# Kernel optimization log

Measured on AMD Instinct MI355X. Metric: run time of the kernel, lower is better.

The kernel has to match this reference:

```python
import jax, jax.numpy as jnp
import numpy as np

EMBED_DIM = 512
BLOCK = 511
N_HEAD = 8
N_GLOBAL = 4
N_LOCAL = 2
N_MIX = 2
RECEP = 4
T = 2 * BLOCK + 2  # [task, clip, BLOCK upper, BLOCK lower]
HD = EMBED_DIM // N_HEAD
NEG = -1e9


def _build_masks():
    bs = BLOCK
    temporal = np.concatenate([np.zeros(2), np.arange(bs) * 2 + 1, np.arange(bs) * 2 + 2])
    seq = temporal[None, :] <= temporal[:, None]  # causal over interleaved temporal order
    tq = np.concatenate([np.arange(bs) * 2 + 1 - 2 * RECEP + 1] * 2)
    tk = np.concatenate([np.arange(bs) * 2 + 1] * 2)
    de = tk[None, :] < tq[:, None]  # keys too far in the past for the sliding window
    local = seq.copy()
    local[2:, 2:] = local[2:, 2:] & ~de
    return jnp.asarray(local), jnp.asarray(seq)


LOCAL_MASK, GLOBAL_MASK = _build_masks()  # (T, T) bool, True = visible


def _linear_params(key, fan_in, fan_out):
    k1, k2 = jax.random.split(key)
    s = 1.0 / np.sqrt(fan_in)
    W = jax.random.uniform(k1, (fan_out, fan_in), minval=-s, maxval=s, dtype=jnp.float32)
    b = jax.random.uniform(k2, (fan_out,), minval=-s, maxval=s, dtype=jnp.float32)
    return W, b


def setup_inputs() -> dict:
    key = jax.random.key(0)
    ks = jax.random.split(key, 10)
    B = 4
    x = jax.random.normal(ks[0], (B, T, EMBED_DIM), dtype=jnp.float32)
    cond_mask = jnp.ones((B, T), dtype=jnp.float32)
    Wq, bq = _linear_params(ks[1], EMBED_DIM, EMBED_DIM)
    Wk, bk = _linear_params(ks[2], EMBED_DIM, EMBED_DIM)
    Wv, bv = _linear_params(ks[3], EMBED_DIM, EMBED_DIM)
    Wqml, bqml = _linear_params(ks[4], EMBED_DIM, HD * N_MIX)
    Wkml, bkml = _linear_params(ks[5], EMBED_DIM, HD * N_MIX)
    Wp, bp = _linear_params(ks[6], EMBED_DIM, EMBED_DIM)
    mix_w = jax.random.normal(ks[7], (N_MIX, 2), dtype=jnp.float32) * 0.5  # Conv2d(2*nm, nm, groups=nm, 1x1)
    bias_clip = jnp.full((1, N_HEAD, 1), 0.5, dtype=jnp.float32)
    bias_clip_ml = jnp.full((1, N_MIX, 1), 0.5, dtype=jnp.float32)
    return dict(x=x, cond_mask=cond_mask, Wq=Wq, bq=bq, Wk=Wk, bk=bk, Wv=Wv, bv=bv,
                Wqml=Wqml, bqml=bqml, Wkml=Wkml, bkml=bkml, mix_w=mix_w, Wp=Wp, bp=bp,
                bias_clip=bias_clip, bias_clip_ml=bias_clip_ml)


def reference(x, cond_mask, Wq, bq, Wk, bk, Wv, bv, Wqml, bqml, Wkml, bkml, mix_w, Wp, bp, bias_clip, bias_clip_ml):
    B, Tx, C = x.shape

    def heads(W, b, nh):
        return (x @ W.T + b).reshape(B, Tx, nh, HD).transpose(0, 2, 1, 3)  # (B, nh, T, hd)

    q = heads(Wq, bq, N_HEAD)
    k = heads(Wk, bk, N_HEAD)
    v = heads(Wv, bv, N_HEAD)
    qml = heads(Wqml, bqml, N_MIX)
    kml = heads(Wkml, bkml, N_MIX)

    scale = 1.0 / np.sqrt(HD)
    # main attention: heads [0:N_LOCAL] local-masked, rest global (causal) masked
    att = jnp.einsum('bhqd,bhkd->bhqk', q, k) * scale
    att = att.at[:, :, :, 1].add(bias_clip)  # learned bias on the CLIP-token key column
    head_mask = jnp.concatenate([
        jnp.broadcast_to(LOCAL_MASK, (N_LOCAL, Tx, Tx)),
        jnp.broadcast_to(GLOBAL_MASK, (N_MIX + N_GLOBAL, Tx, Tx))], axis=0)
    att = jax.nn.softmax(jnp.where(head_mask[None], att, NEG), axis=-1)

    # extra local-masked score maps for the mix heads
    aml = jnp.einsum('bhqd,bhkd->bhqk', qml, kml) * scale
    aml = aml.at[:, :, :, 1].add(bias_clip_ml)
    aml = jax.nn.softmax(jnp.where(LOCAL_MASK[None, None], aml, NEG), axis=-1)

    # grouped 1x1 conv: per mix head, blend (global, local) attention maps
    mix_in = jnp.stack([att[:, N_LOCAL:N_LOCAL + N_MIX], aml], axis=2)  # (B, nm, 2, T, T)
    mix_out = jnp.einsum('ho,bhoqk->bhqk', mix_w, mix_in)

    att_f = jnp.concatenate([att[:, :N_LOCAL], mix_out, att[:, N_LOCAL + N_MIX:]], axis=1)
    y = jnp.einsum('bhqk,bhkd->bhqd', att_f, v)
    y = y.transpose(0, 2, 1, 3).reshape(B, Tx, C)
    return y @ Wp.T + bp
```

## Files before the change

### kernel.cpp

```cpp
#include <hip/hip_runtime.h>

typedef unsigned short u16;
typedef __attribute__((ext_vector_type(8))) __bf16 bf16x8;
typedef __attribute__((ext_vector_type(4))) float f32x4;
typedef __attribute__((ext_vector_type(8))) short short8;
typedef __attribute__((ext_vector_type(4))) u16 us4;

#define T_SEQ 1024
#define PW 1280

__device__ __forceinline__ u16 f2bf(float f) {
  unsigned u = __float_as_uint(f);
  u += 0x7fff + ((u >> 16) & 1);
  return (u16)(u >> 16);
}
__device__ __forceinline__ float bf2f(u16 v) {
  return __uint_as_float((unsigned)v << 16);
}

__constant__ u16 GLOB_M[16] = {0x0101,0x0303,0x0707,0x0F0F,0x1F1F,0x3F3F,0x7F7F,0xFFFF,
                               0xFFFF,0x0307,0x070F,0x0F1F,0x1F3F,0x3F7F,0x7FFF,0xFFFF};
__constant__ u16 LOC_M[16]  = {0x0101,0x0303,0x0607,0x0C0D,0x1819,0x3031,0x6061,0xC0C1,
                               0x8183,0x0307,0x060F,0x0C1D,0x1839,0x3071,0x60E1,0xC1C1};

__device__ __forceinline__ void gll16(const u16* gp, u16* lp) {
  __builtin_amdgcn_global_load_lds((const __attribute__((address_space(1))) unsigned*)gp,
                                   (__attribute__((address_space(3))) unsigned*)lp, 16, 0, 0);
}

template<int NISS>
__device__ __forceinline__ void stage_sw(u16* lds, const u16* __restrict__ g,
                                         int ld, int tid) {
  const int w = tid >> 6;
#pragma unroll
  for (int i = 0; i < NISS; ++i) {
    int row = i * 32 + (tid >> 3);
    int cswz = ((tid & 7) << 4) ^ ((row & 7) << 4);
    gll16(g + (size_t)row * ld + (cswz >> 1), lds + i * 2048 + w * 512);
  }
}

__device__ __forceinline__ bf16x8 rd_sw(const u16* lds, int row, int colbyte) {
  return *(const bf16x8*)&lds[row * 64 + ((colbyte ^ ((row & 7) << 4)) >> 1)];
}

__global__ void prep_all(const float4* __restrict__ x, u16* __restrict__ xb,
                         const float* __restrict__ Wq, const float* __restrict__ Wk,
                         const float* __restrict__ Wv, const float* __restrict__ Wqml,
                         const float* __restrict__ Wkml, const float* __restrict__ Wp,
                         const float* __restrict__ bq, const float* __restrict__ bk,
                         const float* __restrict__ bv, const float* __restrict__ bqml,
                         const float* __restrict__ bkml,
                         u16* __restrict__ Wcat, u16* __restrict__ Wpx, float* __restrict__ bcat) {
  if (blockIdx.x < 2048) {
    int i = blockIdx.x * 256 + threadIdx.x;
    float4 v = x[i];
    us4 o = { f2bf(v.x), f2bf(v.y), f2bf(v.z), f2bf(v.w) };
    *(us4*)&xb[i * 4] = o;
    return;
  }
  int idx = (blockIdx.x - 2048) * 256 + threadIdx.x;
  const int NW = 1792 * 512;
  if (idx < NW) {
    int row = idx >> 9;
    float v;
    if (row < 512)       v = Wq[idx];
    else if (row < 1024) v = Wk[idx - 512 * 512];
    else if (row < 1536) v = Wv[idx - 1024 * 512];
    else if (row < 1664) v = Wqml[idx - 1536 * 512];
    else                 v = Wkml[idx - 1664 * 512];
    Wcat[idx] = f2bf(v);
    return;
  }
  int i2 = idx - NW;
  if (i2 < 512 * 640) {
    int n = i2 / 640, k2 = i2 - n * 640;
    float v = (k2 < 512) ? Wp[n * 512 + k2] : Wp[n * 512 + k2 - 384];
    Wpx[i2] = f2bf(v);
    return;
  }
  int i3 = i2 - 512 * 640;
  if (i3 < 1792) {
    float v;
    if (i3 < 512)       v = bq[i3];
    else if (i3 < 1024) v = bk[i3 - 512];
    else if (i3 < 1536) v = bv[i3 - 1024];
    else if (i3 < 1664) v = bqml[i3 - 1536];
    else                v = bkml[i3 - 1664];
    bcat[i3] = v;
  }
}

__global__ __launch_bounds__(256) void gemm_qkv(
    const u16* __restrict__ A, const u16* __restrict__ Bw,
    const float* __restrict__ bias, u16* __restrict__ Pout, u16* __restrict__ Vtb) {
  __shared__ u16 As[2][8192];
  __shared__ u16 Bs[2][8192];
  const int tid = threadIdx.x;
  const int lane = tid & 63, w = tid >> 6;
  const int g = lane >> 4, c = lane & 15;
  const int n0 = blockIdx.x * 128, m0 = blockIdx.y * 128;
  const int wm = (w >> 1) * 64, wn = (w & 1) * 64;

  f32x4 acc[4][4] = {};
  stage_sw<4>(As[0], A + (size_t)m0 * 512, 512, tid);
  stage_sw<4>(Bs[0], Bw + (size_t)n0 * 512, 512, tid);
  __syncthreads();
  for (int ks = 0; ks < 8; ++ks) {
    int cur = ks & 1;
    if (ks + 1 < 8) {
      stage_sw<4>(As[cur ^ 1], A + (size_t)m0 * 512 + (ks + 1) * 64, 512, tid);
      stage_sw<4>(Bs[cur ^ 1], Bw + (size_t)n0 * 512 + (ks + 1) * 64, 512, tid);
    }
#pragma unroll
    for (int h = 0; h < 2; ++h) {
      bf16x8 av[4], bv[4];
#pragma unroll
      for (int f = 0; f < 4; ++f) {
        av[f] = rd_sw(As[cur], wm + f * 16 + c, h * 64 + g * 16);
        bv[f] = rd_sw(Bs[cur], wn + f * 16 + c, h * 64 + g * 16);
      }
#pragma unroll
      for (int fm = 0; fm < 4; ++fm)
#pragma unroll
        for (int fn = 0; fn < 4; ++fn)
          acc[fm][fn] = __builtin_amdgcn_mfma_f32_16x16x32_bf16(av[fm], bv[fn], acc[fm][fn], 0, 0, 0);
    }
    __syncthreads();
  }

  const bool isV = (n0 >= 1024 && n0 < 1536);
#pragma unroll
  for (int fm = 0; fm < 4; ++fm)
#pragma unroll
    for (int fn = 0; fn < 4; ++fn) {
      int row = m0 + wm + fm * 16 + g * 4;
      int col = n0 + wn + fn * 16 + c;
      float bb = bias[col];
      if (isV) {
        int d = col - 1024;
        int bidx = row >> 10, t = row & 1023;
        us4 pack = { f2bf(acc[fm][fn][0] + bb), f2bf(acc[fm][fn][1] + bb),
                     f2bf(acc[fm][fn][2] + bb), f2bf(acc[fm][fn][3] + bb) };
        *(us4*)&Vtb[((size_t)bidx * 512 + d) * 1024 + t] = pack;
      } else {
        int pcol = (col < 1024) ? col : col - 512;
#pragma unroll
        for (int r = 0; r < 4; ++r)
          Pout[(size_t)(row + r) * PW + pcol] = f2bf(acc[fm][fn][r] + bb);
      }
    }
}

__global__ __launch_bounds__(256) void gemm_out(
    const u16* __restrict__ A, const u16* __restrict__ Bw,
    const float* __restrict__ bias, float* __restrict__ Cout) {
  __shared__ u16 As[2][8192];
  __shared__ u16 Bs[2][4096];
  const int tid = threadIdx.x;
  const int lane = tid & 63, w = tid >> 6;
  const int g = lane >> 4, c = lane & 15;
  const int n0 = blockIdx.x * 64, m0 = blockIdx.y * 128;
  const int wm = (w >> 1) * 64, wn = (w & 1) * 32;

  f32x4 acc[4][2] = {};
  stage_sw<4>(As[0], A + (size_t)m0 * 640, 640, tid);
  stage_sw<2>(Bs[0], Bw + (size_t)n0 * 640, 640, tid);
  __syncthreads();
  for (int ks = 0; ks < 10; ++ks) {
    int cur = ks & 1;
    if (ks + 1 < 10) {
      stage_sw<4>(As[cur ^ 1], A + (size_t)m0 * 640 + (ks + 1) * 64, 640, tid);
      stage_sw<2>(Bs[cur ^ 1], Bw + (size_t)n0 * 640 + (ks + 1) * 64, 640, tid);
    }
#pragma unroll
    for (int h = 0; h < 2; ++h) {
      bf16x8 av[4], bv[2];
#pragma unroll
      for (int f = 0; f < 4; ++f)
        av[f] = rd_sw(As[cur], wm + f * 16 + c, h * 64 + g * 16);
#pragma unroll
      for (int f = 0; f < 2; ++f)
        bv[f] = rd_sw(Bs[cur], wn + f * 16 + c, h * 64 + g * 16);
#pragma unroll
      for (int fm = 0; fm < 4; ++fm)
#pragma unroll
        for (int fn = 0; fn < 2; ++fn)
          acc[fm][fn] = __builtin_amdgcn_mfma_f32_16x16x32_bf16(av[fm], bv[fn], acc[fm][fn], 0, 0, 0);
    }
    __syncthreads();
  }
#pragma unroll
  for (int fm = 0; fm < 4; ++fm)
#pragma unroll
    for (int fn = 0; fn < 2; ++fn)
#pragma unroll
      for (int r = 0; r < 4; ++r) {
        int row = m0 + wm + fm * 16 + g * 4 + r;
        int col = n0 + wn + fn * 16 + c;
        Cout[(size_t)row * 512 + col] = acc[fm][fn][r] + bias[col];
      }
}

__global__ __launch_bounds__(256) void attn_k(
    const u16* __restrict__ P, const u16* __restrict__ Vtb, u16* __restrict__ Y,
    u16* __restrict__ Part_o, float* __restrict__ Part_ml,
    const float* __restrict__ mix_w, const float* __restrict__ bias_clip,
    const float* __restrict__ bias_clip_ml) {
  __shared__ u16 Ks[4096];
  __shared__ u16 Ps[4][16 * 72];
  const int tid = threadIdx.x, lane = tid & 63, w = tid >> 6;
  const int g = lane >> 4, c = lane & 15;
  const int qt = blockIdx.x, u = blockIdx.y, b = blockIdx.z;

  int qcol, kcol, vsel, outcol = 0, slot = -1;
  bool localMask = false;
  float kbias, wgt = 1.0f;
  unsigned mask;
  if (u < 24) {
    int h = 2 + (u >> 2), sp = u & 3; slot = u;
    qcol = h * 64; kcol = 512 + h * 64; vsel = h; kbias = bias_clip[h];
    mask = (unsigned)GLOB_M[qt] & (0x1111u << sp);
  } else if (u < 26) {
    int h = u - 24;
    qcol = h * 64; kcol = 512 + h * 64; vsel = h; outcol = h * 64;
    localMask = true; kbias = bias_clip[h];
    mask = LOC_M[qt];
  } else {
    int mh = u - 26;
    qcol = 1024 + mh * 64; kcol = 1152 + mh * 64; vsel = 2 + mh; outcol = 512 + mh * 64;
    localMask = true; kbias = bias_clip_ml[mh]; wgt = mix_w[mh * 2 + 1];
    mask = LOC_M[qt];
  }
  const size_t baseP = (size_t)b * T_SEQ * PW;
  const u16* __restrict__ Kbase = P + baseP + kcol;
  const u16* __restrict__ Vbase = Vtb + ((size_t)b * 512 + vsel * 64) * 1024;
  const int r0 = qt * 64 + w * 16;
  const int qg = r0 + c;

  int tq = (qg < 2) ? 0 : ((qg < 513) ? 2 * qg - 3 : 2 * qg - 1024);
  int upmax = (tq - 1) >> 1;
  int lomax = (tq - 2) >> 1;
  int wmin = (localMask && qg >= 2) ? ((qg < 513 ? qg - 2 : qg - 513) - 3) : -1000000;

  float mM = -1e8f, lL = 0.0f;
  f32x4 o[4] = {};

  if (mask) {
    bf16x8 aq0 = *(const bf16x8*)&P[baseP + (size_t)qg * PW + qcol + g * 8];
    bf16x8 aq1 = *(const bf16x8*)&P[baseP + (size_t)qg * PW + qcol + 32 + g * 8];

    unsigned rem = mask;
    int kt = __ffs(rem) - 1; rem &= rem - 1;

    for (;;) {
      const int k0 = kt * 64;
      bf16x8 vr[2][4];
#pragma unroll
      for (int ks2 = 0; ks2 < 2; ++ks2)
#pragma unroll
        for (int db = 0; db < 4; ++db)
          vr[ks2][db] = *(const bf16x8*)&Vbase[(size_t)(db * 16 + c) * 1024 + k0 + ks2 * 32 + g * 8];
      stage_sw<2>(Ks, Kbase + (size_t)k0 * PW, PW, tid);
      __syncthreads();

      float s[4][4];
#pragma unroll
      for (int cb = 0; cb < 4; ++cb) {
        f32x4 accs = {};
        bf16x8 bk0 = rd_sw(Ks, cb * 16 + c, g * 16);
        bf16x8 bk1 = rd_sw(Ks, cb * 16 + c, 64 + g * 16);
        accs = __builtin_amdgcn_mfma_f32_16x16x32_bf16(bk0, aq0, accs, 0, 0, 0);
        accs = __builtin_amdgcn_mfma_f32_16x16x32_bf16(bk1, aq1, accs, 0, 0, 0);
#pragma unroll
        for (int r = 0; r < 4; ++r) s[cb][r] = accs[r] * 0.125f;
      }
      __syncthreads();

#pragma unroll
      for (int cb = 0; cb < 4; ++cb) {
        int kb = k0 + cb * 16 + g * 4;
#pragma unroll
        for (int r = 0; r < 4; ++r) {
          int kk = kb + r;
          bool tok = kk < 2;
          bool low = kk >= 513;
          int jk = kk - (low ? 513 : 2);
          int bnd = low ? lomax : upmax;
          bool vis = tok | ((jk <= bnd) & (jk >= wmin));
          float addb = (kk == 1) ? kbias : 0.0f;
          s[cb][r] = vis ? (s[cb][r] + addb) : -1e9f;
        }
      }

      float rmax = s[0][0];
#pragma unroll
      for (int cb = 0; cb < 4; ++cb)
#pragma unroll
        for (int r = 0; r < 4; ++r) rmax = fmaxf(rmax, s[cb][r]);
      rmax = fmaxf(rmax, __shfl_xor(rmax, 16));
      rmax = fmaxf(rmax, __shfl_xor(rmax, 32));
      float mnew = fmaxf(mM, rmax);
      float fr = __expf(mM - mnew);
      float psum = 0.0f;
#pragma unroll
      for (int cb = 0; cb < 4; ++cb)
#pragma unroll
        for (int r = 0; r < 4; ++r) {
          float p = __expf(s[cb][r] - mnew);
          s[cb][r] = p;
          psum += p;
        }
      psum += __shfl_xor(psum, 16);
      psum += __shfl_xor(psum, 32);
      lL = lL * fr + psum;
      mM = mnew;
#pragma unroll
      for (int db = 0; db < 4; ++db) o[db] *= fr;

#pragma unroll
      for (int cb = 0; cb < 4; ++cb) {
        us4 pk = { f2bf(s[cb][0]), f2bf(s[cb][1]), f2bf(s[cb][2]), f2bf(s[cb][3]) };
        *(us4*)&Ps[w][c * 72 + cb * 16 + g * 4] = pk;
      }
      asm volatile("s_waitcnt lgkmcnt(0)" ::: "memory");
      __builtin_amdgcn_sched_barrier(0);

#pragma unroll
      for (int ks2 = 0; ks2 < 2; ++ks2) {
        bf16x8 ap = *(const bf16x8*)&Ps[w][c * 72 + ks2 * 32 + g * 8];
#pragma unroll
        for (int db = 0; db < 4; ++db)
          o[db] = __builtin_amdgcn_mfma_f32_16x16x32_bf16(vr[ks2][db], ap, o[db], 0, 0, 0);
      }

      if (!rem) break;
      kt = __ffs(rem) - 1; rem &= rem - 1;
    }
  }

  if (slot >= 0) {
    u16* po = Part_o + ((size_t)(slot * 4 + b)) * T_SEQ * 64;
#pragma unroll
    for (int db = 0; db < 4; ++db) {
      us4 pk = { f2bf(o[db][0]), f2bf(o[db][1]), f2bf(o[db][2]), f2bf(o[db][3]) };
      *(us4*)&po[(size_t)qg * 64 + db * 16 + g * 4] = pk;
    }
    if (g == 0) {
      float2 ml = { mM, lL };
      *(float2*)&Part_ml[(((size_t)(slot * 4 + b)) * T_SEQ + qg) * 2] = ml;
    }
  } else {
    float wl = wgt / lL;
#pragma unroll
    for (int db = 0; db < 4; ++db) {
      us4 pk = { f2bf(o[db][0] * wl), f2bf(o[db][1] * wl),
                 f2bf(o[db][2] * wl), f2bf(o[db][3] * wl) };
      *(us4*)&Y[((size_t)b * T_SEQ + qg) * 640 + outcol + db * 16 + g * 4] = pk;
    }
  }
}

__global__ __launch_bounds__(256) void combine_k(
    const u16* __restrict__ Part_o, const float* __restrict__ Part_ml,
    u16* __restrict__ Y, const float* __restrict__ mix_w) {
  int idx = blockIdx.x * 256 + threadIdx.x;
  int q4 = idx & 15;
  int row = (idx >> 4) & 1023;
  int bb = (idx >> 14) & 3;
  int hp = idx >> 16;
  float mv[4], lv[4];
  float ms = -1e30f;
#pragma unroll
  for (int s = 0; s < 4; ++s) {
    size_t base = (((size_t)(hp * 4 + s) * 4 + bb) * 1024 + row) * 2;
    mv[s] = Part_ml[base];
    lv[s] = Part_ml[base + 1];
    ms = fmaxf(ms, mv[s]);
  }
  float denom = 0.0f, e[4];
#pragma unroll
  for (int s = 0; s < 4; ++s) { e[s] = __expf(mv[s] - ms); denom += lv[s] * e[s]; }
  float wgt = (hp < 2) ? mix_w[hp * 2] : 1.0f;
  float inv = wgt / denom;
  float out[4] = {0.f, 0.f, 0.f, 0.f};
#pragma unroll
  for (int s = 0; s < 4; ++s) {
    us4 ov = *(const us4*)&Part_o[(((size_t)(hp * 4 + s) * 4 + bb) * 1024 + row) * 64 + q4 * 4];
#pragma unroll
    for (int j = 0; j < 4; ++j) out[j] += e[s] * bf2f(ov[j]);
  }
  us4 pk = { f2bf(out[0] * inv), f2bf(out[1] * inv), f2bf(out[2] * inv), f2bf(out[3] * inv) };
  *(us4*)&Y[((size_t)bb * 1024 + row) * 640 + (hp + 2) * 64 + q4 * 4] = pk;
}

extern "C" void kernel_launch(void* const* d_in, const int* in_sizes, int n_in,
                              void* d_out, int out_size, void* d_ws, size_t ws_size,
                              hipStream_t stream) {
  const float* x     = (const float*)d_in[0];
  const float* Wq    = (const float*)d_in[2];
  const float* bq    = (const float*)d_in[3];
  const float* Wk    = (const float*)d_in[4];
  const float* bk    = (const float*)d_in[5];
  const float* Wv    = (const float*)d_in[6];
  const float* bv    = (const float*)d_in[7];
  const float* Wqml  = (const float*)d_in[8];
  const float* bqml  = (const float*)d_in[9];
  const float* Wkml  = (const float*)d_in[10];
  const float* bkml  = (const float*)d_in[11];
  const float* mixw  = (const float*)d_in[12];
  const float* Wp    = (const float*)d_in[13];
  const float* bp    = (const float*)d_in[14];
  const float* bclip = (const float*)d_in[15];
  const float* bclipml = (const float*)d_in[16];

  u16* xb   = (u16*)d_ws;
  u16* Wcat = xb + 4096 * 512;
  u16* Wpx  = Wcat + 1792 * 512;
  u16* Ybuf = Wpx + 512 * 640;
  u16* Vtb  = Ybuf + 4096 * 640;
  u16* Pbuf = Vtb + 4 * 512 * 1024;
  float* bcat = (float*)(Pbuf + 4096 * 1280);
  u16* Part_o = (u16*)(bcat + 2048);
  float* Part_ml = (float*)(Part_o + 24 * 4 * 1024 * 64);

  prep_all<<<6919, 256, 0, stream>>>((const float4*)x, xb, Wq, Wk, Wv, Wqml, Wkml, Wp,
                                     bq, bk, bv, bqml, bkml, Wcat, Wpx, bcat);
  gemm_qkv<<<dim3(14, 32), 256, 0, stream>>>(xb, Wcat, bcat, Pbuf, Vtb);
  attn_k<<<dim3(16, 28, 4), 256, 0, stream>>>(Pbuf, Vtb, Ybuf, Part_o, Part_ml,
                                              mixw, bclip, bclipml);
  combine_k<<<1536, 256, 0, stream>>>(Part_o, Part_ml, Ybuf, mixw);
  gemm_out<<<dim3(8, 32), 256, 0, stream>>>(Ybuf, Wpx, bp, (float*)d_out);
}
```

Measured before the change: 88.68 us.

## Double-buffer K/V tiles in LDS and enlarge attention blocks to 128 queries

The attention kernel now uses 512-thread blocks covering 128 query rows, so each staged K/V tile is shared by twice as many queries. K and V tiles are both loaded asynchronously into double-buffered LDS, which overlaps the next tile's load with compute on the current one, and V is read from LDS instead of straight from global memory into registers. The cost is a union of two masks per block, which can add tiles that half the rows do not need, plus more LDS per block and half as many blocks to occupy the GPU.

Result: faster. 80.65 us (-9.1%).

```diff
diff --git a/kernel.cpp b/kernel.cpp
--- a/kernel.cpp
+++ b/kernel.cpp
@@ -38,6 +38,13 @@
     int cswz = ((tid & 7) << 4) ^ ((row & 7) << 4);
     gll16(g + (size_t)row * ld + (cswz >> 1), lds + i * 2048 + w * 512);
   }
+}
+
+__device__ __forceinline__ void stage8(u16* lds, const u16* __restrict__ g,
+                                       int ld, int tid) {
+  int row = tid >> 3;
+  int cswz = (((tid & 7) << 4) ^ ((row & 7) << 4)) >> 1;
+  gll16(g + (size_t)row * ld + cswz, lds + (tid >> 6) * 512);
 }
 
 __device__ __forceinline__ bf16x8 rd_sw(const u16* lds, int row, int colbyte) {
@@ -202,16 +209,17 @@
       }
 }
 
-__global__ __launch_bounds__(256) void attn_k(
+__global__ __launch_bounds__(512, 6) void attn_k(
     const u16* __restrict__ P, const u16* __restrict__ Vtb, u16* __restrict__ Y,
     u16* __restrict__ Part_o, float* __restrict__ Part_ml,
     const float* __restrict__ mix_w, const float* __restrict__ bias_clip,
     const float* __restrict__ bias_clip_ml) {
-  __shared__ u16 Ks[4096];
-  __shared__ u16 Ps[4][16 * 72];
+  __shared__ u16 Ks[2][4096];
+  __shared__ u16 Vs[2][4096];
+  __shared__ u16 Ps[8][1152];
   const int tid = threadIdx.x, lane = tid & 63, w = tid >> 6;
   const int g = lane >> 4, c = lane & 15;
-  const int qt = blockIdx.x, u = blockIdx.y, b = blockIdx.z;
+  const int qt2 = blockIdx.x, u = blockIdx.y, b = blockIdx.z;
 
   int qcol, kcol, vsel, outcol = 0, slot = -1;
   bool localMask = false;
@@ -220,22 +228,22 @@
   if (u < 24) {
     int h = 2 + (u >> 2), sp = u & 3; slot = u;
     qcol = h * 64; kcol = 512 + h * 64; vsel = h; kbias = bias_clip[h];
-    mask = (unsigned)GLOB_M[qt] & (0x1111u << sp);
+    mask = ((unsigned)GLOB_M[2 * qt2] | (unsigned)GLOB_M[2 * qt2 + 1]) & (0x1111u << sp);
   } else if (u < 26) {
     int h = u - 24;
     qcol = h * 64; kcol = 512 + h * 64; vsel = h; outcol = h * 64;
     localMask = true; kbias = bias_clip[h];
-    mask = LOC_M[qt];
+    mask = (unsigned)LOC_M[2 * qt2] | (unsigned)LOC_M[2 * qt2 + 1];
   } else {
     int mh = u - 26;
     qcol = 1024 + mh * 64; kcol = 1152 + mh * 64; vsel = 2 + mh; outcol = 512 + mh * 64;
     localMask = true; kbias = bias_clip_ml[mh]; wgt = mix_w[mh * 2 + 1];
-    mask = LOC_M[qt];
+    mask = (unsigned)LOC_M[2 * qt2] | (unsigned)LOC_M[2 * qt2 + 1];
   }
   const size_t baseP = (size_t)b * T_SEQ * PW;
   const u16* __restrict__ Kbase = P + baseP + kcol;
   const u16* __restrict__ Vbase = Vtb + ((size_t)b * 512 + vsel * 64) * 1024;
-  const int r0 = qt * 64 + w * 16;
+  const int r0 = qt2 * 128 + w * 16;
   const int qg = r0 + c;
 
   int tq = (qg < 2) ? 0 : ((qg < 513) ? 2 * qg - 3 : 2 * qg - 1024);
@@ -251,31 +259,36 @@
     bf16x8 aq1 = *(const bf16x8*)&P[baseP + (size_t)qg * PW + qcol + 32 + g * 8];
 
     unsigned rem = mask;
-    int kt = __ffs(rem) - 1; rem &= rem - 1;
+    int kt_cur = __ffs(rem) - 1; rem &= rem - 1;
+    stage8(Ks[0], Kbase + (size_t)(kt_cur * 64) * PW, PW, tid);
+    stage8(Vs[0], Vbase + kt_cur * 64, 1024, tid);
+    int kt_nxt = -1;
+    if (rem) {
+      kt_nxt = __ffs(rem) - 1; rem &= rem - 1;
+      stage8(Ks[1], Kbase + (size_t)(kt_nxt * 64) * PW, PW, tid);
+      stage8(Vs[1], Vbase + kt_nxt * 64, 1024, tid);
+    }
+    int cur = 0;
 
     for (;;) {
-      const int k0 = kt * 64;
-      bf16x8 vr[2][4];
-#pragma unroll
-      for (int ks2 = 0; ks2 < 2; ++ks2)
-#pragma unroll
-        for (int db = 0; db < 4; ++db)
-          vr[ks2][db] = *(const bf16x8*)&Vbase[(size_t)(db * 16 + c) * 1024 + k0 + ks2 * 32 + g * 8];
-      stage_sw<2>(Ks, Kbase + (size_t)k0 * PW, PW, tid);
-      __syncthreads();
+      if (kt_nxt >= 0) asm volatile("s_waitcnt vmcnt(2)" ::: "memory");
+      else             asm volatile("s_waitcnt vmcnt(0)" ::: "memory");
+      __builtin_amdgcn_sched_barrier(0);
+      __builtin_amdgcn_s_barrier();
+
+      const int k0 = kt_cur * 64;
 
       float s[4][4];
 #pragma unroll
       for (int cb = 0; cb < 4; ++cb) {
         f32x4 accs = {};
-        bf16x8 bk0 = rd_sw(Ks, cb * 16 + c, g * 16);
-        bf16x8 bk1 = rd_sw(Ks, cb * 16 + c, 64 + g * 16);
+        bf16x8 bk0 = rd_sw(Ks[cur], cb * 16 + c, g * 16);
+        bf16x8 bk1 = rd_sw(Ks[cur], cb * 16 + c, 64 + g * 16);
         accs = __builtin_amdgcn_mfma_f32_16x16x32_bf16(bk0, aq0, accs, 0, 0, 0);
         accs = __builtin_amdgcn_mfma_f32_16x16x32_bf16(bk1, aq1, accs, 0, 0, 0);
 #pragma unroll
         for (int r = 0; r < 4; ++r) s[cb][r] = accs[r] * 0.125f;
       }
-      __syncthreads();
 
 #pragma unroll
       for (int cb = 0; cb < 4; ++cb) {
@@ -330,12 +343,21 @@
       for (int ks2 = 0; ks2 < 2; ++ks2) {
         bf16x8 ap = *(const bf16x8*)&Ps[w][c * 72 + ks2 * 32 + g * 8];
 #pragma unroll
-        for (int db = 0; db < 4; ++db)
-          o[db] = __builtin_amdgcn_mfma_f32_16x16x32_bf16(vr[ks2][db], ap, o[db], 0, 0, 0);
-      }
-
-      if (!rem) break;
-      kt = __ffs(rem) - 1; rem &= rem - 1;
+        for (int db = 0; db < 4; ++db) {
+          bf16x8 av = rd_sw(Vs[cur], db * 16 + c, ks2 * 64 + g * 16);
+          o[db] = __builtin_amdgcn_mfma_f32_16x16x32_bf16(av, ap, o[db], 0, 0, 0);
+        }
+      }
+
+      __builtin_amdgcn_s_barrier();
+      if (kt_nxt < 0) break;
+      int kt_nn = -1;
+      if (rem) {
+        kt_nn = __ffs(rem) - 1; rem &= rem - 1;
+        stage8(Ks[cur], Kbase + (size_t)(kt_nn * 64) * PW, PW, tid);
+        stage8(Vs[cur], Vbase + kt_nn * 64, 1024, tid);
+      }
+      kt_cur = kt_nxt; kt_nxt = kt_nn; cur ^= 1;
     }
   }
 
@@ -427,8 +449,8 @@
   prep_all<<<6919, 256, 0, stream>>>((const float4*)x, xb, Wq, Wk, Wv, Wqml, Wkml, Wp,
                                      bq, bk, bv, bqml, bkml, Wcat, Wpx, bcat);
   gemm_qkv<<<dim3(14, 32), 256, 0, stream>>>(xb, Wcat, bcat, Pbuf, Vtb);
-  attn_k<<<dim3(16, 28, 4), 256, 0, stream>>>(Pbuf, Vtb, Ybuf, Part_o, Part_ml,
-                                              mixw, bclip, bclipml);
+  attn_k<<<dim3(8, 28, 4), 512, 0, stream>>>(Pbuf, Vtb, Ybuf, Part_o, Part_ml,
+                                             mixw, bclip, bclipml);
   combine_k<<<1536, 256, 0, stream>>>(Part_o, Part_ml, Ybuf, mixw);
   gemm_out<<<dim3(8, 32), 256, 0, stream>>>(Ybuf, Wpx, bp, (float*)d_out);
 }
```
